# Kernel optimization log

Hardware: AMD Instinct MI355X
Metric: run time of the kernel (lower is better)

## Reference

```python
import jax, jax.numpy as jnp
import numpy as np
from functools import partial

STRIDES = (8, 16, 32)
SCORE_THRESH = 0.3
NMS_THRESH = 0.5
TOPK = 500          # fixed pre-NMS candidate count (jit-friendly substitute for boolean masking)
CLASS_OFFSET = 1e4  # offset boxes per class so cross-class IoU == 0 -> per-class NMS


def _decode(cls, reg, obj, stride):
    # cls [B,C,H,W], reg [B,4,H,W], obj [B,1,H,W]
    B, C, H, W = cls.shape
    yv, xv = jnp.meshgrid(jnp.arange(H, dtype=cls.dtype), jnp.arange(W, dtype=cls.dtype), indexing='ij')
    scores = jax.nn.sigmoid(obj) * jax.nn.sigmoid(cls)          # [B,C,H,W]
    dx, dy, dw, dh = reg[:, 0], reg[:, 1], reg[:, 2], reg[:, 3]
    cx = (xv + jax.nn.sigmoid(dx)) * stride
    cy = (yv + jax.nn.sigmoid(dy)) * stride
    w = jnp.exp(dw) * stride
    h = jnp.exp(dh) * stride
    boxes = jnp.stack([cx - w / 2, cy - h / 2, cx + w / 2, cy + h / 2], axis=-1)  # [B,H,W,4]
    return boxes.reshape(B, H * W, 4), scores.reshape(B, C, H * W).transpose(0, 2, 1)


def _pairwise_iou(boxes):
    # boxes [B,K,4] xyxy -> iou [B,K,K]
    area = (boxes[..., 2] - boxes[..., 0]) * (boxes[..., 3] - boxes[..., 1])
    x1 = jnp.maximum(boxes[:, :, None, 0], boxes[:, None, :, 0])
    y1 = jnp.maximum(boxes[:, :, None, 1], boxes[:, None, :, 1])
    x2 = jnp.minimum(boxes[:, :, None, 2], boxes[:, None, :, 2])
    y2 = jnp.minimum(boxes[:, :, None, 3], boxes[:, None, :, 3])
    inter = jnp.clip(x2 - x1, 0) * jnp.clip(y2 - y1, 0)
    union = area[:, :, None] + area[:, None, :] - inter
    return inter / (union + 1e-7)


def _greedy_nms(iou, valid):
    # iou [B,K,K], valid [B,K] -> keep [B,K]; greedy over score-sorted order (axis 1)
    B, K = valid.shape
    def step(supp, i):
        keep_i = valid[:, i] & ~supp[:, i]                    # [B]
        supp = supp | (keep_i[:, None] & (iou[:, i, :] >= NMS_THRESH))
        return supp, keep_i
    _, keep_t = jax.lax.scan(step, jnp.zeros((B, K), dtype=bool), jnp.arange(K))
    return keep_t.T  # [B,K]


def _predict(levels):
    boxes_l, scores_l = [], []
    for (c, r, o), s in zip(levels, STRIDES):
        b, sc = _decode(c, r, o, s)
        boxes_l.append(b)
        scores_l.append(sc)
    boxes = jnp.concatenate(boxes_l, axis=1)     # [B,N,4]
    scores = jnp.concatenate(scores_l, axis=1)   # [B,N,C]
    max_scores = scores.max(axis=-1)             # [B,N]
    labels = jnp.argmax(scores, axis=-1)         # [B,N]
    masked = jnp.where(max_scores > SCORE_THRESH, max_scores, -1.0)
    top_scores, idx = jax.lax.top_k(masked, TOPK)                         # sorted desc
    top_boxes = jnp.take_along_axis(boxes, idx[..., None], axis=1)        # [B,K,4]
    top_labels = jnp.take_along_axis(labels, idx, axis=1)                 # [B,K]
    valid = top_scores > SCORE_THRESH
    boxes_off = top_boxes + (top_labels.astype(top_boxes.dtype) * CLASS_OFFSET)[..., None]
    keep = _greedy_nms(_pairwise_iou(boxes_off), valid)                   # [B,K]
    out_boxes = jnp.where(keep[..., None], top_boxes, 0.0)
    out_scores = jnp.where(keep, top_scores, 0.0)
    return out_boxes, out_scores, top_labels, keep


def setup_inputs() -> dict:
    key = jax.random.key(0)
    ks = jax.random.split(key, 9)
    B, C = 64, 2
    shapes = {
        'cls_p3': (B, C, 160, 160), 'reg_p3': (B, 4, 160, 160), 'obj_p3': (B, 1, 160, 160),
        'cls_p4': (B, C, 80, 80),   'reg_p4': (B, 4, 80, 80),   'obj_p4': (B, 1, 80, 80),
        'cls_p5': (B, C, 40, 40),   'reg_p5': (B, 4, 40, 40),   'obj_p5': (B, 1, 40, 40),
    }
    return {name: jax.random.normal(k, shp, dtype=jnp.float32)
            for k, (name, shp) in zip(ks, shapes.items())}


def reference(cls_p3, reg_p3, obj_p3, cls_p4, reg_p4, obj_p4, cls_p5, reg_p5, obj_p5):
    levels = [(cls_p3, reg_p3, obj_p3), (cls_p4, reg_p4, obj_p4), (cls_p5, reg_p5, obj_p5)]
    return _predict(levels)
```

## Files before the change

kernel.cpp:

```cpp
#include <hip/hip_runtime.h>
#include <hip/hip_bf16.h>
#include <stdint.h>

#define NB 64
#define NA 33600
#define NK 500
#define HW3 25600
#define HW4 6400
#define HW5 1600
#define OFF4 25600
#define OFF5 32000
#define NA4 8400
#define NSEG 33
#define NBIN 256
#define LCAP 1024
#define MROWS 512

typedef unsigned short u16;
typedef unsigned int u32;
typedef unsigned long long u64;

__device__ __forceinline__ float sigf(float x) { return 1.0f / (1.0f + expf(-x)); }

__device__ __forceinline__ u32 f2key(float f) {
  u32 u = __float_as_uint(f);
  return (u & 0x80000000u) ? ~u : (u | 0x80000000u);
}
__device__ __forceinline__ float key2f(u32 k) {
  u32 u = (k & 0x80000000u) ? (k ^ 0x80000000u) : ~k;
  return __uint_as_float(u);
}
__device__ __forceinline__ int bin_of(float s) {
  int b = (int)(s * 256.0f);
  return b > 255 ? 255 : b;
}
__device__ __forceinline__ u32 mkkey(float o, float c0, float c1) {
  float so = sigf(o);
  float s = fmaxf(so * sigf(c0), so * sigf(c1));
  float masked = (s > 0.3f) ? s : -1.0f;
  return f2key(masked);
}
__device__ __forceinline__ u64 uniform64(u64 v) {
  u32 lo = (u32)__builtin_amdgcn_readfirstlane((int)(u32)v);
  u32 hi = (u32)__builtin_amdgcn_readfirstlane((int)(u32)(v >> 32));
  return ((u64)hi << 32) | lo;
}

__global__ __launch_bounds__(256) void k_score(
    const float* __restrict__ cls3, const float* __restrict__ obj3,
    const float* __restrict__ cls4, const float* __restrict__ obj4,
    const float* __restrict__ cls5, const float* __restrict__ obj5,
    uint4* __restrict__ keys4, u16* __restrict__ ghist_part, u32* __restrict__ cnt)
{
  int seg = blockIdx.x, b = blockIdx.y, tid = threadIdx.x;
  int i4 = seg * 256 + tid;
  __shared__ u32 hist[NBIN];
  hist[tid] = 0;
  if (seg == 0 && tid == 0) cnt[b] = 0;
  __syncthreads();

  if (i4 < NA4) {
    const float* cls; const float* obj; int p4, HW;
    if (i4 < 6400)      { cls = cls3; obj = obj3; p4 = i4;        HW = HW3; }
    else if (i4 < 8000) { cls = cls4; obj = obj4; p4 = i4 - 6400; HW = HW4; }
    else                { cls = cls5; obj = obj5; p4 = i4 - 8000; HW = HW5; }
    float4 o  = reinterpret_cast<const float4*>(obj + (size_t)b * HW)[p4];
    float4 c0 = reinterpret_cast<const float4*>(cls + (size_t)(b * 2) * HW)[p4];
    float4 c1 = reinterpret_cast<const float4*>(cls + (size_t)(b * 2 + 1) * HW)[p4];
    uint4 kv;
    kv.x = mkkey(o.x, c0.x, c1.x);
    kv.y = mkkey(o.y, c0.y, c1.y);
    kv.z = mkkey(o.z, c0.z, c1.z);
    kv.w = mkkey(o.w, c0.w, c1.w);
    keys4[(size_t)b * NA4 + i4] = kv;
    u32 ks[4] = {kv.x, kv.y, kv.z, kv.w};
#pragma unroll
    for (int c = 0; c < 4; ++c) {
      float s = key2f(ks[c]);
      if (s > 0.3f) atomicAdd(&hist[bin_of(s)], 1u);
    }
  }
  __syncthreads();
  if (tid < 128) {
    u32 pk = (hist[2 * tid] & 0xFFFFu) | (hist[2 * tid + 1] << 16);
    reinterpret_cast<u32*>(ghist_part + ((size_t)(b * NSEG + seg) * NBIN))[tid] = pk;
  }
}

__global__ __launch_bounds__(256) void k_collect(
    const u32* __restrict__ keys, const u16* __restrict__ ghist_part,
    u64* __restrict__ cand, u32* __restrict__ cnt)
{
  int seg = blockIdx.x, b = blockIdx.y, tid = threadIdx.x;
  __shared__ u32 part[NBIN];
  __shared__ int sh_p;
  __shared__ u64 loc[1024];
  __shared__ u32 lcnt;
  __shared__ u32 gbase;

  u32 sum = 0;
  for (int s2 = 0; s2 < NSEG; ++s2)
    sum += ghist_part[(size_t)(b * NSEG + s2) * NBIN + tid];
  part[tid] = sum;
  if (tid == 0) lcnt = 0;
  __syncthreads();
  for (int off = 1; off < NBIN; off <<= 1) {
    u32 add = (tid + off < NBIN) ? part[tid + off] : 0u;
    __syncthreads();
    part[tid] += add;
    __syncthreads();
  }
  if (tid == 0 && part[0] < NK) sh_p = NBIN;
  u32 S = part[tid];
  u32 Snext = (tid == NBIN - 1) ? 0u : part[tid + 1];
  if (S >= NK && Snext < NK) sh_p = tid;
  __syncthreads();
  int p = sh_p;

  int i4 = seg * 256 + tid;
  if (i4 < NA4) {
    uint4 kv = reinterpret_cast<const uint4*>(keys + (size_t)b * NA)[i4];
    u32 ks[4] = {kv.x, kv.y, kv.z, kv.w};
#pragma unroll
    for (int c = 0; c < 4; ++c) {
      float s = key2f(ks[c]);
      if (s > 0.3f && bin_of(s) >= p) {
        u32 slot = atomicAdd(&lcnt, 1u);
        loc[slot] = ((u64)ks[c] << 16) | (u32)(0xFFFF - (i4 * 4 + c));
      }
    }
  }
  __syncthreads();
  if (tid == 0) gbase = atomicAdd(&cnt[b], lcnt);
  __syncthreads();
  u32 n = lcnt, gb = gbase;
  for (u32 i = tid; i < n; i += 256) {
    u32 slot = gb + i;
    if (slot < LCAP) cand[(size_t)b * LCAP + slot] = loc[i];
  }
}

__global__ __launch_bounds__(512) void k_sortdec(
    const u32* __restrict__ keys, const u64* __restrict__ gcand,
    const u32* __restrict__ cnt,
    const float* __restrict__ cls3, const float* __restrict__ obj3, const float* __restrict__ reg3,
    const float* __restrict__ cls4, const float* __restrict__ obj4, const float* __restrict__ reg4,
    const float* __restrict__ cls5, const float* __restrict__ obj5, const float* __restrict__ reg5,
    float* __restrict__ top_score,
    float4* __restrict__ boxes, float4* __restrict__ boxesoff,
    float* __restrict__ out_labels)
{
  int b = blockIdx.x, tid = threadIdx.x;
  __shared__ u64 cand[LCAP];
  __shared__ int idx_lds[NK];
  __shared__ float score_lds[NK];
  __shared__ u32 hist[256];
  __shared__ u32 part[256];
  __shared__ u32 sh_R;
  __shared__ int sh_digit;
  __shared__ u32 sh_cnt;

  u32 n = cnt[b];
  bool fail = (n < (u32)NK) || (n > LCAP);
  const u32* kb = keys + (size_t)b * NA;

  if (!fail) {
    for (int i = tid; i < LCAP; i += 512)
      cand[i] = (i < (int)n) ? gcand[(size_t)b * LCAP + i] : 0ull;
    for (int k = 2; k <= LCAP; k <<= 1) {
      for (int j = k >> 1; j > 0; j >>= 1) {
        __syncthreads();
        int i = ((tid & ~(j - 1)) << 1) | (tid & (j - 1));
        int ixj = i | j;
        u64 a = cand[i], c2 = cand[ixj];
        bool dir = ((i & k) == 0);
        if ((a < c2) == dir) { cand[i] = c2; cand[ixj] = a; }
      }
    }
    __syncthreads();
    if (tid < NK) {
      u64 kk = cand[tid];
      idx_lds[tid] = 0xFFFF - (int)(kk & 0xFFFFull);
      score_lds[tid] = key2f((u32)(kk >> 16));
    }
  } else {
    u64 prefix = 0, prefmask = 0;
    u32 R = NK;
    for (int pass = 0; pass < 6; ++pass) {
      int shift = 40 - 8 * pass;
      if (tid < 256) part[tid] = 0;
      __syncthreads();
      for (int i = tid; i < NA; i += 512) {
        u64 k48 = ((u64)kb[i] << 16) | (u32)(0xFFFF - i);
        if ((k48 & prefmask) == prefix)
          atomicAdd(&part[(u32)(k48 >> shift) & 255u], 1u);
      }
      __syncthreads();
      if (tid < 256) hist[tid] = part[tid];
      __syncthreads();
      for (int off = 1; off < 256; off <<= 1) {
        u32 add = 0;
        if (tid < 256 && tid + off < 256) add = hist[tid + off];
        __syncthreads();
        if (tid < 256) hist[tid] += add;
        __syncthreads();
      }
      if (tid < 256) {
        u32 s = hist[tid];
        u32 snext = (tid == 255) ? 0u : hist[tid + 1];
        if (s >= R && snext < R) { sh_digit = tid; sh_R = R - snext; }
      }
      __syncthreads();
      prefix |= ((u64)sh_digit) << shift;
      R = sh_R;
      prefmask |= 0xFFull << shift;
      __syncthreads();
    }
    if (tid == 0) sh_cnt = 0;
    if (tid < NK) { idx_lds[tid] = 0; score_lds[tid] = -1.0f; }
    __syncthreads();
    for (int i = tid; i < NA; i += 512) {
      u64 k48 = ((u64)kb[i] << 16) | (u32)(0xFFFF - i);
      if (k48 >= prefix) {
        u32 slot = atomicAdd(&sh_cnt, 1u);
        if (slot < 512) cand[slot] = k48;
      }
    }
    __syncthreads();
    int m = (sh_cnt < (u32)NK) ? (int)sh_cnt : NK;
    for (int t = tid; t < m; t += 512) {
      u64 k = cand[t];
      int rank = 0;
      for (int j = 0; j < m; ++j) rank += (cand[j] > k) ? 1 : 0;
      if (rank < NK) {
        idx_lds[rank] = 0xFFFF - (int)(k & 0xFFFFull);
        score_lds[rank] = key2f((u32)(k >> 16));
      }
    }
  }
  __syncthreads();

  if (tid < NK) {
    int a = idx_lds[tid];
    const float *cls, *obj, *reg; int pos, HW, x, y; float stride;
    if (a < OFF4) {
      cls = cls3; obj = obj3; reg = reg3; pos = a; HW = HW3; stride = 8.0f;
      y = pos / 160; x = pos - y * 160;
    } else if (a < OFF5) {
      cls = cls4; obj = obj4; reg = reg4; pos = a - OFF4; HW = HW4; stride = 16.0f;
      y = pos / 80; x = pos - y * 80;
    } else {
      cls = cls5; obj = obj5; reg = reg5; pos = a - OFF5; HW = HW5; stride = 32.0f;
      y = pos / 40; x = pos - y * 40;
    }
    float dx = reg[(b * 4 + 0) * HW + pos];
    float dy = reg[(b * 4 + 1) * HW + pos];
    float dw = reg[(b * 4 + 2) * HW + pos];
    float dh = reg[(b * 4 + 3) * HW + pos];
    float cx = ((float)x + sigf(dx)) * stride;
    float cy = ((float)y + sigf(dy)) * stride;
    float w = expf(dw) * stride;
    float h = expf(dh) * stride;
    float x1 = cx - w * 0.5f, y1 = cy - h * 0.5f;
    float x2 = cx + w * 0.5f, y2 = cy + h * 0.5f;
    float so = sigf(obj[b * HW + pos]);
    float s0 = so * sigf(cls[(b * 2) * HW + pos]);
    float s1 = so * sigf(cls[(b * 2 + 1) * HW + pos]);
    int label = (s1 > s0) ? 1 : 0;
    float off = (float)label * 10000.0f;
    int t = b * NK + tid;
    boxes[t]    = make_float4(x1, y1, x2, y2);
    boxesoff[t] = make_float4(x1 + off, y1 + off, x2 + off, y2 + off);
    out_labels[t] = (float)label;
    top_score[t] = score_lds[tid];
  }
}

__global__ __launch_bounds__(256) void k_iou(
    const float4* __restrict__ boxesoff, u64* __restrict__ mask)
{
  int t = blockIdx.x * 256 + threadIdx.x;
  if (t >= NB * NK * 8) return;
  int w = t & 7;
  int bi = t >> 3;
  int b = bi / NK;
  int i = bi - b * NK;
  float4 A = boxesoff[bi];
  float areaA = (A.z - A.x) * (A.w - A.y);
  const float4* base = boxesoff + b * NK;
  int j0 = w * 64;
  int jmax = (NK - j0 < 64) ? (NK - j0) : 64;
  u64 bits = 0;
  for (int jj = 0; jj < jmax; ++jj) {
    float4 Bx = base[j0 + jj];
    float areaB = (Bx.z - Bx.x) * (Bx.w - Bx.y);
    float ix1 = fmaxf(A.x, Bx.x);
    float iy1 = fmaxf(A.y, Bx.y);
    float ix2 = fminf(A.z, Bx.z);
    float iy2 = fminf(A.w, Bx.w);
    float iw = fmaxf(ix2 - ix1, 0.0f);
    float ih = fmaxf(iy2 - iy1, 0.0f);
    float inter = iw * ih;
    float uni = areaA + areaB - inter;
    float iou = inter / (uni + 1e-7f);
    bits |= ((u64)(iou >= 0.5f)) << jj;
  }
  mask[(size_t)b * (MROWS * 8) + (size_t)i * 8 + w] = bits;
}

__global__ __launch_bounds__(64) void k_nms(
    const u64* __restrict__ mask, const float* __restrict__ top_score,
    const float4* __restrict__ boxes,
    float* __restrict__ out_boxes, float* __restrict__ out_scores,
    float* __restrict__ out_keep)
{
  int b = blockIdx.x;
  int lane = threadIdx.x;
  const u64* mb = mask + (size_t)b * (MROWS * 8);

  u64 rw[8][8];
#pragma unroll
  for (int c = 0; c < 8; ++c) {
    const ulonglong2* rp =
        reinterpret_cast<const ulonglong2*>(mb + (size_t)(c * 64 + lane) * 8);
#pragma unroll
    for (int q = 0; q < 4; ++q) {
      ulonglong2 v = rp[q];
      rw[c][2 * q] = v.x;
      rw[c][2 * q + 1] = v.y;
    }
  }

  u64 validw[8];
#pragma unroll
  for (int c = 0; c < 8; ++c) {
    int r = c * 64 + lane;
    float s = (r < NK) ? top_score[b * NK + r] : -1.0f;
    validw[c] = __ballot(s > 0.3f);
  }

  u64 himask = (lane == 63) ? 0ull : (~0ull << (lane + 1));
  u64 k[8];
#pragma unroll
  for (int w = 0; w < 8; ++w) k[w] = validw[w];

  for (int it = 0; it < 600; ++it) {
    u64 acc[8] = {0, 0, 0, 0, 0, 0, 0, 0};
#pragma unroll
    for (int c = 0; c < 8; ++c) {
      u64 msel = 0ull - ((k[c] >> lane) & 1ull);
      acc[c] |= rw[c][c] & himask & msel;
#pragma unroll
      for (int w = c + 1; w < 8; ++w) acc[w] |= rw[c][w] & msel;
    }
#pragma unroll
    for (int off = 1; off < 64; off <<= 1) {
#pragma unroll
      for (int w = 0; w < 8; ++w)
        acc[w] |= (u64)__shfl_xor((unsigned long long)acc[w], off, 64);
    }
    bool conv = true;
#pragma unroll
    for (int w = 0; w < 8; ++w) {
      u64 nk = validw[w] & ~uniform64(acc[w]);
      conv = conv && (nk == k[w]);
      k[w] = nk;
    }
    if (conv) break;
  }

#pragma unroll
  for (int c = 0; c < 8; ++c) {
    int r = c * 64 + lane;
    if (r < NK) {
      int kp = (int)((k[c] >> lane) & 1ull);
      float4 bx = boxes[b * NK + r];
      float s = top_score[b * NK + r];
      float4 ob;
      ob.x = kp ? bx.x : 0.0f;
      ob.y = kp ? bx.y : 0.0f;
      ob.z = kp ? bx.z : 0.0f;
      ob.w = kp ? bx.w : 0.0f;
      reinterpret_cast<float4*>(out_boxes)[b * NK + r] = ob;
      out_scores[b * NK + r] = kp ? s : 0.0f;
      out_keep[b * NK + r]   = kp ? 1.0f : 0.0f;
    }
  }
}

extern "C" void kernel_launch(void* const* d_in, const int* in_sizes, int n_in,
                              void* d_out, int out_size, void* d_ws, size_t ws_size,
                              hipStream_t stream) {
  const float* cls3 = (const float*)d_in[0];
  const float* reg3 = (const float*)d_in[1];
  const float* obj3 = (const float*)d_in[2];
  const float* cls4 = (const float*)d_in[3];
  const float* reg4 = (const float*)d_in[4];
  const float* obj4 = (const float*)d_in[5];
  const float* cls5 = (const float*)d_in[6];
  const float* reg5 = (const float*)d_in[7];
  const float* obj5 = (const float*)d_in[8];

  char* ws = (char*)d_ws;
  u32*    keys      = (u32*)   (ws + 0);
  u16*    ghist     = (u16*)   (ws + 8601600);
  u32*    cnt       = (u32*)   (ws + 9682944);
  u64*    cand      = (u64*)   (ws + 9683200);
  float*  top_score = (float*) (ws + 10207488);
  float4* boxes     = (float4*)(ws + 10335488);
  float4* boxesoff  = (float4*)(ws + 10847488);
  u64*    mask      = (u64*)   (ws + 11359488);

  float* out        = (float*)d_out;
  float* out_boxes  = out;
  float* out_scores = out + 128000;
  float* out_labels = out + 160000;
  float* out_keep   = out + 192000;

  dim3 gfull(NSEG, NB);
  k_score<<<gfull, 256, 0, stream>>>(cls3, obj3, cls4, obj4, cls5, obj5,
                                     (uint4*)keys, ghist, cnt);
  k_collect<<<gfull, 256, 0, stream>>>(keys, ghist, cand, cnt);
  k_sortdec<<<NB, 512, 0, stream>>>(keys, cand, cnt,
      cls3, obj3, reg3, cls4, obj4, reg4, cls5, obj5, reg5,
      top_score, boxes, boxesoff, out_labels);
  k_iou<<<(NB * NK * 8 + 255) / 256, 256, 0, stream>>>(boxesoff, mask);
  k_nms<<<NB, 64, 0, stream>>>(mask, top_score, boxes, out_boxes, out_scores, out_keep);
}
```

Baseline: 89.20 us.

## Replace bitonic sort with rank sort and skip lower-triangle IoU mask words

In the top-K selection, the bitonic sort over 1024 candidates is replaced by a rank-counting sort: each candidate counts how many keys exceed it and scatters itself to that rank when below K. This removes the many barrier-separated sort stages, at the cost of O(n^2) LDS compares per block. The IoU kernel also skips mask words whose 64-column block lies entirely below the row's block, and the NMS kernel loads only the upper-triangular words. The intent is to cut sync overhead and IoU work, relying on NMS reading only forward suppression bits.

```diff
diff --git a/kernel.cpp b/kernel.cpp
--- a/kernel.cpp
+++ b/kernel.cpp
@@ -165,23 +165,17 @@
   const u32* kb = keys + (size_t)b * NA;
 
   if (!fail) {
-    for (int i = tid; i < LCAP; i += 512)
-      cand[i] = (i < (int)n) ? gcand[(size_t)b * LCAP + i] : 0ull;
-    for (int k = 2; k <= LCAP; k <<= 1) {
-      for (int j = k >> 1; j > 0; j >>= 1) {
-        __syncthreads();
-        int i = ((tid & ~(j - 1)) << 1) | (tid & (j - 1));
-        int ixj = i | j;
-        u64 a = cand[i], c2 = cand[ixj];
-        bool dir = ((i & k) == 0);
-        if ((a < c2) == dir) { cand[i] = c2; cand[ixj] = a; }
-      }
-    }
+    for (int i = tid; i < (int)n; i += 512)
+      cand[i] = gcand[(size_t)b * LCAP + i];
     __syncthreads();
-    if (tid < NK) {
-      u64 kk = cand[tid];
-      idx_lds[tid] = 0xFFFF - (int)(kk & 0xFFFFull);
-      score_lds[tid] = key2f((u32)(kk >> 16));
+    for (int t = tid; t < (int)n; t += 512) {
+      u64 kk = cand[t];
+      int rank = 0;
+      for (int j = 0; j < (int)n; ++j) rank += (cand[j] > kk) ? 1 : 0;
+      if (rank < NK) {
+        idx_lds[rank] = 0xFFFF - (int)(kk & 0xFFFFull);
+        score_lds[rank] = key2f((u32)(kk >> 16));
+      }
     }
   } else {
     u64 prefix = 0, prefmask = 0;
@@ -285,6 +279,7 @@
   int bi = t >> 3;
   int b = bi / NK;
   int i = bi - b * NK;
+  if (w < (i >> 6)) return;
   float4 A = boxesoff[bi];
   float areaA = (A.z - A.x) * (A.w - A.y);
   const float4* base = boxesoff + b * NK;
@@ -321,14 +316,10 @@
   u64 rw[8][8];
 #pragma unroll
   for (int c = 0; c < 8; ++c) {
-    const ulonglong2* rp =
-        reinterpret_cast<const ulonglong2*>(mb + (size_t)(c * 64 + lane) * 8);
-#pragma unroll
-    for (int q = 0; q < 4; ++q) {
-      ulonglong2 v = rp[q];
-      rw[c][2 * q] = v.x;
-      rw[c][2 * q + 1] = v.y;
-    }
+    const u64* rp = mb + (size_t)(c * 64 + lane) * 8;
+#pragma unroll
+    for (int w = 0; w < 8; ++w)
+      if (w >= c) rw[c][w] = rp[w];
   }
 
   u64 validw[8];
```

New measurement: 93.03 us. 4.3% more time.
